# Kernel optimization log

Measured on AMD Instinct MI355X. Metric: run time of the kernel, lower is better.

The kernel has to match this reference:

```python
import jax, jax.numpy as jnp
import numpy as np

B, N, D, OUT = 8192, 256, 128, 10  # batch, input_dim (sites), bond_dim, output_dim
LOCAL = 2  # local physical dimension (hardcoded in source)


def setup_inputs() -> dict:
    key = jax.random.key(0)
    ks = jax.random.split(key, 6)
    scale = 1.0 / np.sqrt(D)  # stable variant of source's 0.1 init (keeps 256-site product O(1))
    x = jax.random.normal(ks[0], (B, N), dtype=jnp.float32)
    first = jax.random.normal(ks[1], (1, LOCAL, D), dtype=jnp.float32) * scale   # site 0: (1,2,D)
    mid = jax.random.normal(ks[2], (N - 2, D, LOCAL, D), dtype=jnp.float32) * scale  # sites 1..N-2
    last = jax.random.normal(ks[3], (D, LOCAL, 1), dtype=jnp.float32) * scale    # site N-1: (D,2,1)
    w = jax.random.normal(ks[4], (OUT, 1), dtype=jnp.float32) * 0.1  # nn.Linear(1, OUT) weight
    b = jnp.zeros((OUT,), dtype=jnp.float32)                          # nn.Linear(1, OUT) bias
    return {"x": x, "first": first, "mid": mid, "last": last, "w": w, "b": b}


def _feature_map(x):
    # per-sample min/max normalization over the feature axis, then (cos, sin) embedding
    x_min = jnp.min(x, axis=1, keepdims=True)
    x_max = jnp.max(x, axis=1, keepdims=True)
    x_norm = (x - x_min) / (x_max - x_min + 1e-6)
    ang = (np.pi / 2) * x_norm
    return jnp.stack([jnp.cos(ang), jnp.sin(ang)], axis=2)  # [B, N, 2]


def reference(x, first, mid, last, w, b):
    phi = _feature_map(x)  # [B, N, 2]
    # site 0: left[b, r] = sum_d first[0, d, r] * phi[b, 0, d]
    left = jnp.einsum('dr,bd->br', first[0], phi[:, 0])  # [B, D]
    # sites 1..N-2 via scan: left <- sum_{l,d} left[b,l] * M[l,d,r] * phi[b,i,d]
    phi_mid = jnp.swapaxes(phi[:, 1:-1], 0, 1)  # [N-2, B, 2]

    def step(left, inputs):
        M, p = inputs  # M: [D, 2, D], p: [B, 2]
        left = jnp.einsum('bl,ldr,bd->br', left, M, p)
        return left, None

    left, _ = jax.lax.scan(step, left, (mid, phi_mid))  # [B, D]
    # last site: scalar[b] = sum_{l,d} left[b,l] * last[l,d,0] * phi[b,N-1,d]
    scalar = jnp.einsum('bl,ld,bd->b', left, last[:, :, 0], phi[:, -1])  # [B]
    # nn.Linear(1, OUT): logits = scalar * w^T + b
    logits = scalar[:, None] * w[:, 0][None, :] + b  # [B, OUT]
    return logits
```

## Files before the change

### kernel.cpp

```cpp
#include <hip/hip_runtime.h>


typedef _Float16 v8h __attribute__((ext_vector_type(8)));
typedef _Float16 h2  __attribute__((ext_vector_type(2)));
typedef float    v4f __attribute__((ext_vector_type(4)));

#define PI_HALF 1.5707963267948966f
#define SITE_U4 4096
#define TOFF_U4 (127*4096)

union U4H8 { uint4 u; v8h h; };

__device__ __forceinline__ v4f mfma16h(uint4 a, uint4 b, v4f c){
  U4H8 ua, ub; ua.u = a; ub.u = b;
  return __builtin_amdgcn_mfma_f32_16x16x32_f16(ua.h, ub.h, c, 0, 0, 0);
}
__device__ __forceinline__ unsigned pack2h(float lo, float hi){
  h2 p; p[0] = (_Float16)lo; p[1] = (_Float16)hi;
  return __builtin_bit_cast(unsigned, p);
}
__device__ __forceinline__ unsigned short f16b(float v){
  return __builtin_bit_cast(unsigned short, (_Float16)v);
}

__global__ __launch_bounds__(256) void repack_mid(const float* __restrict__ mid,
                                                  unsigned short* __restrict__ wsB){
  const int bid = blockIdx.x;
  if (bid < 508){
    int idx  = bid * 256 + threadIdx.x;
    int lg   = idx & 15;
    int nt   = (idx >> 4) & 7;
    int kt   = (idx >> 7) & 3;
    int d    = (idx >> 9) & 1;
    int site = idx >> 10;
    int q    = lg >> 2;
    int n0   = 16*nt + 4*(lg & 3);
    const float* src = mid + ((size_t)(site*128 + 32*kt + 8*q)*2 + d)*128 + n0;
    float V[8][4];
    #pragma unroll
    for (int j = 0; j < 8; ++j){
      float4 a = *(const float4*)(src + (size_t)j*256);
      V[j][0]=a.x; V[j][1]=a.y; V[j][2]=a.z; V[j][3]=a.w;
    }
    uint4* dst = (uint4*)wsB + ((((size_t)site*2 + d)*4 + kt)*8 + nt)*64
               + 16*q + 4*(lg & 3);
    #pragma unroll
    for (int t = 0; t < 4; ++t){
      uint4 o;
      o.x = pack2h(V[0][t], V[1][t]);
      o.y = pack2h(V[2][t], V[3][t]);
      o.z = pack2h(V[4][t], V[5][t]);
      o.w = pack2h(V[6][t], V[7][t]);
      dst[t] = o;
    }
  } else {
    int idx  = (bid - 508) * 256 + threadIdx.x;
    int lg   = idx & 15;
    int kt   = (idx >> 4) & 3;
    int am   = (idx >> 6) & 7;
    int d    = (idx >> 9) & 1;
    int srel = idx >> 10;
    int site = 127 + srel;
    int q    = lg >> 2;
    int m0   = 16*am + 4*(lg & 3);
    int k0   = 32*kt + 8*q;
    uint4* dst = (uint4*)wsB + TOFF_U4
               + ((((size_t)srel*2 + d)*8 + am)*4 + kt)*64 + 16*q + 4*(lg & 3);
    #pragma unroll
    for (int mp = 0; mp < 4; ++mp){
      const float* src = mid + ((size_t)((site*128 + m0 + mp)*2) + d)*128 + k0;
      float4 a = *(const float4*)(src);
      float4 b = *(const float4*)(src + 4);
      uint4 o;
      o.x = pack2h(a.x, a.y);
      o.y = pack2h(a.z, a.w);
      o.z = pack2h(b.x, b.y);
      o.w = pack2h(b.z, b.w);
      dst[mp] = o;
    }
  }
}

__global__ __launch_bounds__(1024, 4) void mps_main(
    const float* __restrict__ x,
    const float* __restrict__ first,
    const unsigned short* __restrict__ wsBv,
    const float* __restrict__ lastw,
    const float* __restrict__ wlin,
    const float* __restrict__ blin,
    float* __restrict__ out)
{
  __shared__ unsigned phiT[256*36];
  __shared__ unsigned Af[2*8*64*4];
  __shared__ unsigned Rf[2*8*64*4];
  __shared__ float Rcomb[128*33];
  __shared__ float scal[32];

  const int tid  = threadIdx.x;
  const int gblk = blockIdx.x;
  const int w    = tid >> 6;
  const int lane = tid & 63;
  const int r    = lane & 15;
  const int q    = lane >> 4;
  const int rh   = r >> 3;
  const int rowbase = gblk * 32;
  const int physL = lane ^ ((lane >> 3) & 7);

  {
    const int row = tid >> 5;
    const int c0  = (tid & 31) * 8;
    const float4* xp = (const float4*)(x + (size_t)(rowbase + row) * 256 + c0);
    float xv[8];
    float vmin = 3.0e38f, vmax = -3.0e38f;
    #pragma unroll
    for (int c = 0; c < 2; ++c){
      float4 u = xp[c];
      xv[c*4+0] = u.x; xv[c*4+1] = u.y; xv[c*4+2] = u.z; xv[c*4+3] = u.w;
      vmin = fminf(vmin, fminf(fminf(u.x,u.y), fminf(u.z,u.w)));
      vmax = fmaxf(vmax, fmaxf(fmaxf(u.x,u.y), fmaxf(u.z,u.w)));
    }
    #pragma unroll
    for (int m = 1; m < 32; m <<= 1){
      vmin = fminf(vmin, __shfl_xor(vmin, m));
      vmax = fmaxf(vmax, __shfl_xor(vmax, m));
    }
    const float sc = PI_HALF / (vmax - vmin + 1e-6f);
    #pragma unroll
    for (int j = 0; j < 8; ++j){
      float a = (xv[j] - vmin) * sc;
      phiT[(c0 + j)*36 + row] = pack2h(__cosf(a), __sinf(a));
    }
  }
  __syncthreads();

  uint4 F0[8], F1[8];
  if (w < 8){
    const int mt = w >> 2, kt = w & 3;
    float f0[8], f1[8];
    #pragma unroll
    for (int j = 0; j < 8; ++j){
      int l = 32*kt + 8*q + j;
      f0[j] = first[l]; f1[j] = first[128 + l];
    }
    h2 p0 = __builtin_bit_cast(h2, phiT[0*36 + 16*mt + r]);
    const float c0 = (float)p0[0], s0 = (float)p0[1];
    uint4 o;
    o.x = pack2h(f0[0]*c0 + f1[0]*s0, f0[1]*c0 + f1[1]*s0);
    o.y = pack2h(f0[2]*c0 + f1[2]*s0, f0[3]*c0 + f1[3]*s0);
    o.z = pack2h(f0[4]*c0 + f1[4]*s0, f0[5]*c0 + f1[5]*s0);
    o.w = pack2h(f0[6]*c0 + f1[6]*s0, f0[7]*c0 + f1[7]*s0);
    *(uint4*)&Af[((mt*4 + kt)*64 + physL)*4] = o;
    const uint4* bp = (const uint4*)wsBv;
    #pragma unroll
    for (int d = 0; d < 2; ++d)
      #pragma unroll
      for (int kk = 0; kk < 4; ++kk)
        F0[d*4+kk] = bp[(size_t)((d*4 + kk)*8 + w)*64 + lane];
  } else {
    const int ww = w - 8;
    const int kt = ww >> 1, nt = ww & 1;
    const int n  = 16*nt + r;
    h2 p5 = __builtin_bit_cast(h2, phiT[255*36 + n]);
    const float cb = (float)p5[0], sb = (float)p5[1];
    uint4 o; unsigned ow[4];
    #pragma unroll
    for (int jp = 0; jp < 4; ++jp){
      const int k = 32*kt + 8*q + 2*jp;
      float2 g0 = *(const float2*)(lastw + 2*k);
      float2 g1 = *(const float2*)(lastw + 2*(k+1));
      ow[jp] = pack2h(g0.x*cb + g0.y*sb, g1.x*cb + g1.y*sb);
    }
    o.x=ow[0]; o.y=ow[1]; o.z=ow[2]; o.w=ow[3];
    *(uint4*)&Rf[((kt*2 + nt)*64 + physL)*4] = o;
    const uint4* bp = (const uint4*)wsBv + TOFF_U4 + (size_t)126 * SITE_U4;
    #pragma unroll
    for (int d = 0; d < 2; ++d)
      #pragma unroll
      for (int kk = 0; kk < 4; ++kk)
        F0[d*4+kk] = bp[(size_t)((d*8 + ww)*4 + kk)*64 + lane];
  }

  auto body = [&](int t, uint4 (&Fc)[8], uint4 (&Fn)[8]){
    __syncthreads();

    if (w < 8){
      {
        const int soff = (t < 126) ? (t + 1) : 0;
        const uint4* bp = (const uint4*)wsBv + (size_t)soff * SITE_U4;
        #pragma unroll
        for (int d = 0; d < 2; ++d)
          #pragma unroll
          for (int kk = 0; kk < 4; ++kk)
            Fn[d*4+kk] = bp[(size_t)((d*4 + kk)*8 + w)*64 + lane];
      }
      v4f ac0[2] = {};
      v4f ac1[2] = {};
      const unsigned* Ab = &Af[(t & 1) * 2048];
      #pragma unroll
      for (int kt = 0; kt < 4; ++kt){
        uint4 a0 = *(const uint4*)&Ab[((0*4 + kt)*64 + physL)*4];
        uint4 a1 = *(const uint4*)&Ab[((1*4 + kt)*64 + physL)*4];
        ac0[0] = mfma16h(a0, Fc[0*4+kt], ac0[0]);
        ac0[1] = mfma16h(a1, Fc[0*4+kt], ac0[1]);
        ac1[0] = mfma16h(a0, Fc[1*4+kt], ac1[0]);
        ac1[1] = mfma16h(a1, Fc[1*4+kt], ac1[1]);
      }
      if (t < 126){
        unsigned short* Wb = (unsigned short*)&Af[((t+1) & 1) * 2048];
        const int X  = 4*(w & 1) + 2*rh + (q >> 1);
        const int S0 = 32*(w & 1) + 16*rh + 4*q;
        #pragma unroll
        for (int mt = 0; mt < 2; ++mt){
          uint4 phiu = *(const uint4*)&phiT[(t+1)*36 + 16*mt + 4*q];
          const unsigned pr[4] = {phiu.x, phiu.y, phiu.z, phiu.w};
          const int base16 = (mt*4 + (w >> 1))*512;
          #pragma unroll
          for (int reg = 0; reg < 4; ++reg){
            h2 ph = __builtin_bit_cast(h2, pr[reg]);
            float v = (float)ph[0]*ac0[mt][reg] + (float)ph[1]*ac1[mt][reg];
            Wb[base16 + ((S0 + reg) ^ X)*8 + (r & 7)] = f16b(v);
          }
        }
      } else {
        float vf[2][4];
        #pragma unroll
        for (int mt = 0; mt < 2; ++mt){
          uint4 phiu = *(const uint4*)&phiT[127*36 + 16*mt + 4*q];
          const unsigned pr[4] = {phiu.x, phiu.y, phiu.z, phiu.w};
          #pragma unroll
          for (int reg = 0; reg < 4; ++reg){
            h2 ph = __builtin_bit_cast(h2, pr[reg]);
            vf[mt][reg] = (float)ph[0]*ac0[mt][reg] + (float)ph[1]*ac1[mt][reg];
          }
        }
        if (tid < 32) scal[tid] = 0.0f;
        __syncthreads();
        float p[2][4] = {};
        const int l = 16*w + r;
        #pragma unroll
        for (int mt = 0; mt < 2; ++mt)
          #pragma unroll
          for (int reg = 0; reg < 4; ++reg)
            p[mt][reg] = vf[mt][reg] * Rcomb[l*33 + 16*mt + 4*q + reg];
        #pragma unroll
        for (int m = 1; m < 16; m <<= 1)
          #pragma unroll
          for (int mt = 0; mt < 2; ++mt)
            #pragma unroll
            for (int reg = 0; reg < 4; ++reg)
              p[mt][reg] += __shfl_xor(p[mt][reg], m);
        if (r == 0){
          #pragma unroll
          for (int mt = 0; mt < 2; ++mt)
            #pragma unroll
            for (int reg = 0; reg < 4; ++reg)
              atomicAdd(&scal[16*mt + 4*q + reg], p[mt][reg]);
        }
      }
    } else {
      const int ww = w - 8;
      {
        const int srel = (t < 126) ? (125 - t) : 0;
        const uint4* bp = (const uint4*)wsBv + TOFF_U4 + (size_t)srel * SITE_U4;
        #pragma unroll
        for (int d = 0; d < 2; ++d)
          #pragma unroll
          for (int kk = 0; kk < 4; ++kk)
            Fn[d*4+kk] = bp[(size_t)((d*8 + ww)*4 + kk)*64 + lane];
      }
      v4f ac0[2] = {};
      v4f ac1[2] = {};
      const unsigned* Rb = &Rf[(t & 1) * 2048];
      #pragma unroll
      for (int kt = 0; kt < 4; ++kt){
        uint4 b0 = *(const uint4*)&Rb[((kt*2 + 0)*64 + physL)*4];
        uint4 b1 = *(const uint4*)&Rb[((kt*2 + 1)*64 + physL)*4];
        ac0[0] = mfma16h(Fc[0*4+kt], b0, ac0[0]);
        ac0[1] = mfma16h(Fc[0*4+kt], b1, ac0[1]);
        ac1[0] = mfma16h(Fc[1*4+kt], b0, ac1[0]);
        ac1[1] = mfma16h(Fc[1*4+kt], b1, ac1[1]);
      }
      const int ps = 254 - t;
      if (t < 126){
        unsigned short* Wr = (unsigned short*)&Rf[((t+1) & 1) * 2048];
        const int X = 4*(ww & 1) + 2*(q >> 1) + rh;
        const int S = (32*(ww & 1) + 16*(q >> 1) + r) ^ X;
        #pragma unroll
        for (int nt = 0; nt < 2; ++nt){
          h2 ph = __builtin_bit_cast(h2, phiT[ps*36 + 16*nt + r]);
          const float cb = (float)ph[0], sb = (float)ph[1];
          const int base = ((ww >> 1)*2 + nt)*512 + S*8 + 4*(q & 1);
          #pragma unroll
          for (int reg = 0; reg < 4; ++reg){
            float v = cb*ac0[nt][reg] + sb*ac1[nt][reg];
            Wr[base + reg] = f16b(v);
          }
        }
      } else {
        #pragma unroll
        for (int nt = 0; nt < 2; ++nt){
          h2 ph = __builtin_bit_cast(h2, phiT[128*36 + 16*nt + r]);
          const float cb = (float)ph[0], sb = (float)ph[1];
          #pragma unroll
          for (int reg = 0; reg < 4; ++reg){
            float v = cb*ac0[nt][reg] + sb*ac1[nt][reg];
            const int l = 16*ww + 4*q + reg;
            Rcomb[l*33 + 16*nt + r] = v;
          }
        }
        if (tid < 32) scal[tid] = 0.0f;
        __syncthreads();
      }
    }

    if (t == 126){
      __syncthreads();
      for (int t2 = tid; t2 < 320; t2 += 1024){
        int bb = t2 / 10, o = t2 - bb*10;
        out[(size_t)(rowbase + bb)*10 + o] = scal[bb]*wlin[o] + blin[o];
      }
    }
  };

  #pragma unroll 1
  for (int t = 0; t < 126; t += 2){
    body(t,     F0, F1);
    body(t + 1, F1, F0);
  }
  body(126, F0, F1);
}

extern "C" void kernel_launch(void* const* d_in, const int* in_sizes, int n_in,
                              void* d_out, int out_size, void* d_ws, size_t ws_size,
                              hipStream_t stream){
  (void)in_sizes; (void)n_in; (void)out_size; (void)ws_size;
  const float* x     = (const float*)d_in[0];
  const float* first = (const float*)d_in[1];
  const float* mid   = (const float*)d_in[2];
  const float* lastw = (const float*)d_in[3];
  const float* wlin  = (const float*)d_in[4];
  const float* blin  = (const float*)d_in[5];
  float* o            = (float*)d_out;
  unsigned short* wsB = (unsigned short*)d_ws;

  hipLaunchKernelGGL(repack_mid, dim3(1016), dim3(256),  0, stream, mid, wsB);
  hipLaunchKernelGGL(mps_main,   dim3(256),  dim3(1024), 0, stream,
                     x, first, wsB, lastw, wlin, blin, o);
}
```

Baseline: 274.2 us.

## Merge forward and backward sweeps into each wave with 512-thread blocks

Instead of devoting 8 waves to the left-to-right chain and 8 to the right-to-left chain in a 1024-thread block, each of 8 waves now runs both chains, issuing both sets of MFMAs and weight prefetches per step. This halves block size and barrier participants and lets each wave interleave two independent MFMA chains to hide latency. In exchange, per-thread register use roughly doubles (two double-buffered fragment sets), which may limit occupancy or cause spills, and the feature-map prologue does twice the work per thread.

```diff
diff --git a/kernel.cpp b/kernel.cpp
--- a/kernel.cpp
+++ b/kernel.cpp
@@ -81,7 +81,7 @@
   }
 }
 
-__global__ __launch_bounds__(1024, 4) void mps_main(
+__global__ __launch_bounds__(512, 2) void mps_main(
     const float* __restrict__ x,
     const float* __restrict__ first,
     const unsigned short* __restrict__ wsBv,
@@ -107,34 +107,33 @@
   const int physL = lane ^ ((lane >> 3) & 7);
 
   {
-    const int row = tid >> 5;
-    const int c0  = (tid & 31) * 8;
+    const int row = tid >> 4;
+    const int c0  = (tid & 15) * 16;
     const float4* xp = (const float4*)(x + (size_t)(rowbase + row) * 256 + c0);
-    float xv[8];
+    float xv[16];
     float vmin = 3.0e38f, vmax = -3.0e38f;
     #pragma unroll
-    for (int c = 0; c < 2; ++c){
+    for (int c = 0; c < 4; ++c){
       float4 u = xp[c];
       xv[c*4+0] = u.x; xv[c*4+1] = u.y; xv[c*4+2] = u.z; xv[c*4+3] = u.w;
       vmin = fminf(vmin, fminf(fminf(u.x,u.y), fminf(u.z,u.w)));
       vmax = fmaxf(vmax, fmaxf(fmaxf(u.x,u.y), fmaxf(u.z,u.w)));
     }
     #pragma unroll
-    for (int m = 1; m < 32; m <<= 1){
+    for (int m = 1; m < 16; m <<= 1){
       vmin = fminf(vmin, __shfl_xor(vmin, m));
       vmax = fmaxf(vmax, __shfl_xor(vmax, m));
     }
     const float sc = PI_HALF / (vmax - vmin + 1e-6f);
     #pragma unroll
-    for (int j = 0; j < 8; ++j){
+    for (int j = 0; j < 16; ++j){
       float a = (xv[j] - vmin) * sc;
       phiT[(c0 + j)*36 + row] = pack2h(__cosf(a), __sinf(a));
     }
   }
   __syncthreads();
 
-  uint4 F0[8], F1[8];
-  if (w < 8){
+  {
     const int mt = w >> 2, kt = w & 3;
     float f0[8], f1[8];
     #pragma unroll
@@ -150,15 +149,9 @@
     o.z = pack2h(f0[4]*c0 + f1[4]*s0, f0[5]*c0 + f1[5]*s0);
     o.w = pack2h(f0[6]*c0 + f1[6]*s0, f0[7]*c0 + f1[7]*s0);
     *(uint4*)&Af[((mt*4 + kt)*64 + physL)*4] = o;
-    const uint4* bp = (const uint4*)wsBv;
-    #pragma unroll
-    for (int d = 0; d < 2; ++d)
-      #pragma unroll
-      for (int kk = 0; kk < 4; ++kk)
-        F0[d*4+kk] = bp[(size_t)((d*4 + kk)*8 + w)*64 + lane];
-  } else {
-    const int ww = w - 8;
-    const int kt = ww >> 1, nt = ww & 1;
+  }
+  {
+    const int kt = w >> 1, nt = w & 1;
     const int n  = 16*nt + r;
     h2 p5 = __builtin_bit_cast(h2, phiT[255*36 + n]);
     const float cb = (float)p5[0], sb = (float)p5[1];
@@ -172,40 +165,80 @@
     }
     o.x=ow[0]; o.y=ow[1]; o.z=ow[2]; o.w=ow[3];
     *(uint4*)&Rf[((kt*2 + nt)*64 + physL)*4] = o;
+  }
+
+  uint4 Ff0[8], Ff1[8], Fb0[8], Fb1[8];
+  {
+    const uint4* bp = (const uint4*)wsBv;
+    #pragma unroll
+    for (int d = 0; d < 2; ++d)
+      #pragma unroll
+      for (int kk = 0; kk < 4; ++kk)
+        Ff0[d*4+kk] = bp[(size_t)((d*4 + kk)*8 + w)*64 + lane];
+  }
+  {
     const uint4* bp = (const uint4*)wsBv + TOFF_U4 + (size_t)126 * SITE_U4;
     #pragma unroll
     for (int d = 0; d < 2; ++d)
       #pragma unroll
       for (int kk = 0; kk < 4; ++kk)
-        F0[d*4+kk] = bp[(size_t)((d*8 + ww)*4 + kk)*64 + lane];
-  }
-
-  auto body = [&](int t, uint4 (&Fc)[8], uint4 (&Fn)[8]){
+        Fb0[d*4+kk] = bp[(size_t)((d*8 + w)*4 + kk)*64 + lane];
+  }
+
+  auto body = [&](int t, uint4 (&FfC)[8], uint4 (&FfN)[8],
+                         uint4 (&FbC)[8], uint4 (&FbN)[8]){
     __syncthreads();
 
-    if (w < 8){
-      {
-        const int soff = (t < 126) ? (t + 1) : 0;
-        const uint4* bp = (const uint4*)wsBv + (size_t)soff * SITE_U4;
-        #pragma unroll
-        for (int d = 0; d < 2; ++d)
-          #pragma unroll
-          for (int kk = 0; kk < 4; ++kk)
-            Fn[d*4+kk] = bp[(size_t)((d*4 + kk)*8 + w)*64 + lane];
-      }
-      v4f ac0[2] = {};
-      v4f ac1[2] = {};
+    {
+      const int soff = (t < 126) ? (t + 1) : 0;
+      const uint4* bp = (const uint4*)wsBv + (size_t)soff * SITE_U4;
+      #pragma unroll
+      for (int d = 0; d < 2; ++d)
+        #pragma unroll
+        for (int kk = 0; kk < 4; ++kk)
+          FfN[d*4+kk] = bp[(size_t)((d*4 + kk)*8 + w)*64 + lane];
+    }
+    {
+      const int srel = (t < 126) ? (125 - t) : 0;
+      const uint4* bp = (const uint4*)wsBv + TOFF_U4 + (size_t)srel * SITE_U4;
+      #pragma unroll
+      for (int d = 0; d < 2; ++d)
+        #pragma unroll
+        for (int kk = 0; kk < 4; ++kk)
+          FbN[d*4+kk] = bp[(size_t)((d*8 + w)*4 + kk)*64 + lane];
+    }
+
+    v4f fa0[2] = {};
+    v4f fa1[2] = {};
+    {
       const unsigned* Ab = &Af[(t & 1) * 2048];
       #pragma unroll
       for (int kt = 0; kt < 4; ++kt){
         uint4 a0 = *(const uint4*)&Ab[((0*4 + kt)*64 + physL)*4];
         uint4 a1 = *(const uint4*)&Ab[((1*4 + kt)*64 + physL)*4];
-        ac0[0] = mfma16h(a0, Fc[0*4+kt], ac0[0]);
-        ac0[1] = mfma16h(a1, Fc[0*4+kt], ac0[1]);
-        ac1[0] = mfma16h(a0, Fc[1*4+kt], ac1[0]);
-        ac1[1] = mfma16h(a1, Fc[1*4+kt], ac1[1]);
-      }
-      if (t < 126){
+        fa0[0] = mfma16h(a0, FfC[0*4+kt], fa0[0]);
+        fa0[1] = mfma16h(a1, FfC[0*4+kt], fa0[1]);
+        fa1[0] = mfma16h(a0, FfC[1*4+kt], fa1[0]);
+        fa1[1] = mfma16h(a1, FfC[1*4+kt], fa1[1]);
+      }
+    }
+    v4f ba0[2] = {};
+    v4f ba1[2] = {};
+    {
+      const unsigned* Rb = &Rf[(t & 1) * 2048];
+      #pragma unroll
+      for (int kt = 0; kt < 4; ++kt){
+        uint4 b0 = *(const uint4*)&Rb[((kt*2 + 0)*64 + physL)*4];
+        uint4 b1 = *(const uint4*)&Rb[((kt*2 + 1)*64 + physL)*4];
+        ba0[0] = mfma16h(FbC[0*4+kt], b0, ba0[0]);
+        ba0[1] = mfma16h(FbC[0*4+kt], b1, ba0[1]);
+        ba1[0] = mfma16h(FbC[1*4+kt], b0, ba1[0]);
+        ba1[1] = mfma16h(FbC[1*4+kt], b1, ba1[1]);
+      }
+    }
+
+    if (t < 126){
+      {
         unsigned short* Wb = (unsigned short*)&Af[((t+1) & 1) * 2048];
         const int X  = 4*(w & 1) + 2*rh + (q >> 1);
         const int S0 = 32*(w & 1) + 16*rh + 4*q;
@@ -217,105 +250,77 @@
           #pragma unroll
           for (int reg = 0; reg < 4; ++reg){
             h2 ph = __builtin_bit_cast(h2, pr[reg]);
-            float v = (float)ph[0]*ac0[mt][reg] + (float)ph[1]*ac1[mt][reg];
+            float v = (float)ph[0]*fa0[mt][reg] + (float)ph[1]*fa1[mt][reg];
             Wb[base16 + ((S0 + reg) ^ X)*8 + (r & 7)] = f16b(v);
           }
         }
-      } else {
-        float vf[2][4];
-        #pragma unroll
-        for (int mt = 0; mt < 2; ++mt){
-          uint4 phiu = *(const uint4*)&phiT[127*36 + 16*mt + 4*q];
-          const unsigned pr[4] = {phiu.x, phiu.y, phiu.z, phiu.w};
+      }
+      {
+        const int ps = 254 - t;
+        unsigned short* Wr = (unsigned short*)&Rf[((t+1) & 1) * 2048];
+        const int X = 4*(w & 1) + 2*(q >> 1) + rh;
+        const int S = (32*(w & 1) + 16*(q >> 1) + r) ^ X;
+        #pragma unroll
+        for (int nt = 0; nt < 2; ++nt){
+          h2 ph = __builtin_bit_cast(h2, phiT[ps*36 + 16*nt + r]);
+          const float cb = (float)ph[0], sb = (float)ph[1];
+          const int base = ((w >> 1)*2 + nt)*512 + S*8 + 4*(q & 1);
           #pragma unroll
           for (int reg = 0; reg < 4; ++reg){
-            h2 ph = __builtin_bit_cast(h2, pr[reg]);
-            vf[mt][reg] = (float)ph[0]*ac0[mt][reg] + (float)ph[1]*ac1[mt][reg];
+            float v = cb*ba0[nt][reg] + sb*ba1[nt][reg];
+            Wr[base + reg] = f16b(v);
           }
         }
-        if (tid < 32) scal[tid] = 0.0f;
-        __syncthreads();
-        float p[2][4] = {};
-        const int l = 16*w + r;
+      }
+    } else {
+      float vf[2][4];
+      #pragma unroll
+      for (int mt = 0; mt < 2; ++mt){
+        uint4 phiu = *(const uint4*)&phiT[127*36 + 16*mt + 4*q];
+        const unsigned pr[4] = {phiu.x, phiu.y, phiu.z, phiu.w};
+        #pragma unroll
+        for (int reg = 0; reg < 4; ++reg){
+          h2 ph = __builtin_bit_cast(h2, pr[reg]);
+          vf[mt][reg] = (float)ph[0]*fa0[mt][reg] + (float)ph[1]*fa1[mt][reg];
+        }
+      }
+      #pragma unroll
+      for (int nt = 0; nt < 2; ++nt){
+        h2 ph = __builtin_bit_cast(h2, phiT[128*36 + 16*nt + r]);
+        const float cb = (float)ph[0], sb = (float)ph[1];
+        #pragma unroll
+        for (int reg = 0; reg < 4; ++reg){
+          float v = cb*ba0[nt][reg] + sb*ba1[nt][reg];
+          const int l = 16*w + 4*q + reg;
+          Rcomb[l*33 + 16*nt + r] = v;
+        }
+      }
+      if (tid < 32) scal[tid] = 0.0f;
+      __syncthreads();
+
+      float p[2][4];
+      const int lcol = 16*w + r;
+      #pragma unroll
+      for (int mt = 0; mt < 2; ++mt)
+        #pragma unroll
+        for (int reg = 0; reg < 4; ++reg)
+          p[mt][reg] = vf[mt][reg] * Rcomb[lcol*33 + 16*mt + 4*q + reg];
+      #pragma unroll
+      for (int m = 1; m < 16; m <<= 1)
         #pragma unroll
         for (int mt = 0; mt < 2; ++mt)
           #pragma unroll
           for (int reg = 0; reg < 4; ++reg)
-            p[mt][reg] = vf[mt][reg] * Rcomb[l*33 + 16*mt + 4*q + reg];
-        #pragma unroll
-        for (int m = 1; m < 16; m <<= 1)
+            p[mt][reg] += __shfl_xor(p[mt][reg], m);
+      if (r == 0){
+        #pragma unroll
+        for (int mt = 0; mt < 2; ++mt)
           #pragma unroll
-          for (int mt = 0; mt < 2; ++mt)
-            #pragma unroll
-            for (int reg = 0; reg < 4; ++reg)
-              p[mt][reg] += __shfl_xor(p[mt][reg], m);
-        if (r == 0){
-          #pragma unroll
-          for (int mt = 0; mt < 2; ++mt)
-            #pragma unroll
-            for (int reg = 0; reg < 4; ++reg)
-              atomicAdd(&scal[16*mt + 4*q + reg], p[mt][reg]);
-        }
-      }
-    } else {
-      const int ww = w - 8;
-      {
-        const int srel = (t < 126) ? (125 - t) : 0;
-        const uint4* bp = (const uint4*)wsBv + TOFF_U4 + (size_t)srel * SITE_U4;
-        #pragma unroll
-        for (int d = 0; d < 2; ++d)
-          #pragma unroll
-          for (int kk = 0; kk < 4; ++kk)
-            Fn[d*4+kk] = bp[(size_t)((d*8 + ww)*4 + kk)*64 + lane];
-      }
-      v4f ac0[2] = {};
-      v4f ac1[2] = {};
-      const unsigned* Rb = &Rf[(t & 1) * 2048];
-      #pragma unroll
-      for (int kt = 0; kt < 4; ++kt){
-        uint4 b0 = *(const uint4*)&Rb[((kt*2 + 0)*64 + physL)*4];
-        uint4 b1 = *(const uint4*)&Rb[((kt*2 + 1)*64 + physL)*4];
-        ac0[0] = mfma16h(Fc[0*4+kt], b0, ac0[0]);
-        ac0[1] = mfma16h(Fc[0*4+kt], b1, ac0[1]);
-        ac1[0] = mfma16h(Fc[1*4+kt], b0, ac1[0]);
-        ac1[1] = mfma16h(Fc[1*4+kt], b1, ac1[1]);
-      }
-      const int ps = 254 - t;
-      if (t < 126){
-        unsigned short* Wr = (unsigned short*)&Rf[((t+1) & 1) * 2048];
-        const int X = 4*(ww & 1) + 2*(q >> 1) + rh;
-        const int S = (32*(ww & 1) + 16*(q >> 1) + r) ^ X;
-        #pragma unroll
-        for (int nt = 0; nt < 2; ++nt){
-          h2 ph = __builtin_bit_cast(h2, phiT[ps*36 + 16*nt + r]);
-          const float cb = (float)ph[0], sb = (float)ph[1];
-          const int base = ((ww >> 1)*2 + nt)*512 + S*8 + 4*(q & 1);
-          #pragma unroll
-          for (int reg = 0; reg < 4; ++reg){
-            float v = cb*ac0[nt][reg] + sb*ac1[nt][reg];
-            Wr[base + reg] = f16b(v);
-          }
-        }
-      } else {
-        #pragma unroll
-        for (int nt = 0; nt < 2; ++nt){
-          h2 ph = __builtin_bit_cast(h2, phiT[128*36 + 16*nt + r]);
-          const float cb = (float)ph[0], sb = (float)ph[1];
-          #pragma unroll
-          for (int reg = 0; reg < 4; ++reg){
-            float v = cb*ac0[nt][reg] + sb*ac1[nt][reg];
-            const int l = 16*ww + 4*q + reg;
-            Rcomb[l*33 + 16*nt + r] = v;
-          }
-        }
-        if (tid < 32) scal[tid] = 0.0f;
-        __syncthreads();
-      }
-    }
-
-    if (t == 126){
+          for (int reg = 0; reg < 4; ++reg)
+            atomicAdd(&scal[16*mt + 4*q + reg], p[mt][reg]);
+      }
       __syncthreads();
-      for (int t2 = tid; t2 < 320; t2 += 1024){
+      for (int t2 = tid; t2 < 320; t2 += 512){
         int bb = t2 / 10, o = t2 - bb*10;
         out[(size_t)(rowbase + bb)*10 + o] = scal[bb]*wlin[o] + blin[o];
       }
@@ -324,10 +329,10 @@
 
   #pragma unroll 1
   for (int t = 0; t < 126; t += 2){
-    body(t,     F0, F1);
-    body(t + 1, F1, F0);
-  }
-  body(126, F0, F1);
+    body(t,     Ff0, Ff1, Fb0, Fb1);
+    body(t + 1, Ff1, Ff0, Fb1, Fb0);
+  }
+  body(126, Ff0, Ff1, Fb0, Fb1);
 }
 
 extern "C" void kernel_launch(void* const* d_in, const int* in_sizes, int n_in,
@@ -343,7 +348,7 @@
   float* o            = (float*)d_out;
   unsigned short* wsB = (unsigned short*)d_ws;
 
-  hipLaunchKernelGGL(repack_mid, dim3(1016), dim3(256),  0, stream, mid, wsB);
-  hipLaunchKernelGGL(mps_main,   dim3(256),  dim3(1024), 0, stream,
+  hipLaunchKernelGGL(repack_mid, dim3(1016), dim3(256), 0, stream, mid, wsB);
+  hipLaunchKernelGGL(mps_main,   dim3(256),  dim3(512), 0, stream,
                      x, first, wsB, lastw, wlin, blin, o);
 }
```

Result: slower. 286.6 us (+4.5%).
